# Performance work log

Hardware: AMD Instinct MI355X
Metric: run time of the kernel (lower is better)

Reference implementation:

```python
import jax, jax.numpy as jnp
import numpy as np
from jax import lax

EPS = 1e-8
ROOT_2 = 1.41421
STYLE_SIZE = 512
OUT_CH = 512
STYLE_SCALE = (2.0 / STYLE_SIZE) ** 0.5   # Weight_Scaling(style_size): equalized-LR sqrt(2/fan_in)
OUT_SCALE = (2.0 / (OUT_CH * 1 * 1)) ** 0.5  # Weight_Scaling(out_channels*1*1)


def setup_inputs() -> dict:
    key = jax.random.key(0)
    ks = jax.random.split(key, 10)
    B, Cin, Cout, H, S = 8, 512, 512, 32, 512
    return {
        "x": jax.random.normal(ks[0], (B, Cin, H, H), dtype=jnp.float32),
        "style_base": jax.random.normal(ks[1], (B, S), dtype=jnp.float32),
        "noise": jax.random.normal(ks[2], (B, 1, 2 * H, 2 * H), dtype=jnp.float32),
        "t": jax.random.normal(ks[3], (B, Cout, 2 * H, 2 * H), dtype=jnp.float32),
        # learned params
        "affine_w": jax.random.normal(ks[4], (Cin, S), dtype=jnp.float32) * (1.0 / np.sqrt(S)),
        "affine_b": jnp.zeros((Cin,), dtype=jnp.float32),
        "conv_w": jax.random.normal(ks[5], (Cout, Cin, 3, 3), dtype=jnp.float32),
        "conv_b": jnp.zeros((1, Cout, 1, 1), dtype=jnp.float32),
        "prelu_a": jnp.asarray(0.25, dtype=jnp.float32),
        "noise_scalar": jnp.zeros((1, Cout, 1, 1), dtype=jnp.float32) + 0.1,
        "out_w": jax.random.normal(ks[6], (3, Cout, 1, 1), dtype=jnp.float32) * (1.0 / np.sqrt(Cout)),
        "out_b": jnp.zeros((3,), dtype=jnp.float32),
    }


def reference(x, style_base, noise, t, affine_w, affine_b, conv_w, conv_b,
              prelu_a, noise_scalar, out_w, out_b):
    B, Cin, H, W = x.shape
    # style_std = affine(Weight_Scaling(style_base)) + 1  -> [B, Cin]
    style_std = (style_base * STYLE_SCALE) @ affine_w.T + affine_b + 1.0

    # bilinear x2 upsample (align_corners=False == half-pixel, matches jax.image.resize)
    x = jax.image.resize(x, (B, Cin, 2 * H, 2 * W), method="bilinear")

    # modulated conv with L2 demodulation, expressed as input-scale + conv + output-scale
    # per-sample weight w_b[o,i,k,l] = w[o,i,k,l]*s[b,i] / ||w*s||_b,o
    wsq = jnp.sum(conv_w ** 2, axis=(2, 3))                      # [O, I]
    demod = 1.0 / jnp.sqrt(jnp.einsum("oi,bi->bo", wsq, style_std ** 2) + EPS)  # [B, O]
    xm = x * style_std[:, :, None, None]
    y = lax.conv_general_dilated(xm, conv_w, (1, 1), "SAME",
                                 dimension_numbers=("NCHW", "OIHW", "NCHW"))
    y = y * demod[:, :, None, None] + conv_b + noise_scalar * noise
    # PReLU (single shared slope)
    y = jnp.where(y >= 0, y, prelu_a * y)

    # out branch: skip add, scale, toRGB 1x1 conv, clamp
    y = (y + t) / ROOT_2
    out = lax.conv_general_dilated(y * OUT_SCALE, out_w, (1, 1), "SAME",
                                   dimension_numbers=("NCHW", "OIHW", "NCHW"))
    out = jnp.clip(out + out_b[None, :, None, None], 0.0, 1.0)
    return (y, out)
```

## Files before the change

kernel.cpp:

```cpp
#include <hip/hip_runtime.h>


typedef short bf16x8 __attribute__((ext_vector_type(8)));
typedef short short8v __attribute__((ext_vector_type(8)));
typedef float f32x16 __attribute__((ext_vector_type(16)));

#define WS_STYLE 0
#define WS_DEMOD 16384
#define WS_WSQ   32768
#define WS_WPACK 1081344
#define WS_XM    5799936
#define WS_PART  41484288

__device__ __forceinline__ short f2bf(float f) {
  unsigned u = __float_as_uint(f);
  u += 0x7FFFu + ((u >> 16) & 1u);
  return (short)(u >> 16);
}

__device__ __forceinline__ void gld16(const short* g, char* l) {
  __builtin_amdgcn_global_load_lds((const __attribute__((address_space(1))) void*)g,
                                   (__attribute__((address_space(3))) void*)l,
                                   16, 0, 0);
}

__global__ void k_style(const float* __restrict__ sb, const float* __restrict__ aw,
                        const float* __restrict__ ab, float* __restrict__ style) {
  __shared__ float s_sb[512];
  int b = blockIdx.x;
  for (int i = threadIdx.x; i < 512; i += 256) s_sb[i] = sb[b * 512 + i] * 0.0625f;
  __syncthreads();
  for (int i = threadIdx.x; i < 512; i += 256) {
    const float4* wrow = (const float4*)(aw + (size_t)i * 512);
    float acc = 0.f;
    #pragma unroll 4
    for (int s4 = 0; s4 < 128; ++s4) {
      float4 w4 = wrow[s4];
      float4 sv = *(const float4*)(s_sb + s4 * 4);
      acc += w4.x * sv.x + w4.y * sv.y + w4.z * sv.z + w4.w * sv.w;
    }
    style[b * 512 + i] = acc + ab[i] + 1.0f;
  }
}

__global__ void k_wsq(const float* __restrict__ cw, float* __restrict__ wsq) {
  int idx = blockIdx.x * 256 + threadIdx.x;
  const float* p = cw + (size_t)idx * 9;
  float s = 0.f;
  #pragma unroll
  for (int j = 0; j < 9; ++j) s += p[j] * p[j];
  wsq[idx] = s;
}

__global__ void k_demod(const float* __restrict__ wsq, const float* __restrict__ style,
                        float* __restrict__ demod) {
  int wid = threadIdx.x >> 6, lane = threadIdx.x & 63;
  int idx = blockIdx.x * 4 + wid;
  int b = idx >> 9, o = idx & 511;
  const float* wr = wsq + (size_t)o * 512;
  const float* ss = style + b * 512;
  float sum = 0.f;
  #pragma unroll
  for (int k = 0; k < 8; ++k) {
    int i = k * 64 + lane;
    float s = ss[i];
    sum += wr[i] * s * s;
  }
  #pragma unroll
  for (int off = 32; off; off >>= 1) sum += __shfl_down(sum, off);
  if (lane == 0) demod[b * 512 + o] = rsqrtf(sum + 1e-8f);
}

__global__ void k_upsample(const float* __restrict__ x, const float* __restrict__ style,
                           short* __restrict__ xm) {
  int b = blockIdx.x / 66, hp = blockIdx.x % 66;
  short* xmp = xm + ((size_t)b * 66 + hp) * 66 * 512;
  if (hp == 0 || hp == 65) {
    short8v z = {0, 0, 0, 0, 0, 0, 0, 0};
    for (int u = threadIdx.x; u < 66 * 512 / 8; u += 256) ((short8v*)xmp)[u] = z;
    return;
  }
  int h = hp - 1;
  int j0 = (h >> 1) - 1 + (h & 1);
  float fj = (h & 1) ? 0.25f : 0.75f;
  int j0c = j0 < 0 ? 0 : j0;
  int j1c = j0 + 1 > 31 ? 31 : j0 + 1;
  __shared__ float xt[2][64][33];
  int ccc = threadIdx.x & 63;
  int wsub = threadIdx.x >> 6;
  for (int c0 = 0; c0 < 512; c0 += 64) {
    __syncthreads();
    #pragma unroll 4
    for (int k = 0; k < 16; ++k) {
      int idx = k * 256 + threadIdx.x;
      int ii = idx & 31, cc = (idx >> 5) & 63, jj = idx >> 11;
      xt[jj][cc][ii] = x[(((size_t)b * 512 + c0 + cc) * 32 + (jj ? j1c : j0c)) * 32 + ii];
    }
    __syncthreads();
    float sstyle = style[b * 512 + c0 + ccc];
    #pragma unroll 4
    for (int wk = 0; wk < 16; ++wk) {
      int w = wk * 4 + wsub;
      int i0 = (w >> 1) - 1 + (w & 1);
      float fi = (w & 1) ? 0.25f : 0.75f;
      int i0c = i0 < 0 ? 0 : i0;
      int i1c = i0 + 1 > 31 ? 31 : i0 + 1;
      float v0 = xt[0][ccc][i0c] * (1.f - fi) + xt[0][ccc][i1c] * fi;
      float v1 = xt[1][ccc][i0c] * (1.f - fi) + xt[1][ccc][i1c] * fi;
      float v = (v0 * (1.f - fj) + v1 * fj) * sstyle;
      xmp[(size_t)(w + 1) * 512 + c0 + ccc] = f2bf(v);
    }
    if (wsub == 0) {
      xmp[c0 + ccc] = 0;
      xmp[(size_t)65 * 512 + c0 + ccc] = 0;
    }
  }
}

__global__ void k_packw(const float* __restrict__ cw, short* __restrict__ wpk) {
  int unit = blockIdx.x * 256 + threadIdx.x;
  int s = unit >> 11;
  int rem = unit & 2047;
  int o = rem >> 2, sp = rem & 3;
  int tap = s >> 4, cc = s & 15;
  int i0 = cc * 32 + ((sp ^ ((o >> 1) & 3)) << 3);
  const float* src = cw + ((size_t)o * 512 + i0) * 9 + tap;
  short8v v;
  #pragma unroll
  for (int j = 0; j < 8; ++j) v[j] = f2bf(src[j * 9]);
  *(short8v*)(wpk + (size_t)unit * 8) = v;
}

__global__ __launch_bounds__(256, 2) void k_conv(
    const short* __restrict__ xm, const short* __restrict__ wpk,
    const float* __restrict__ demod, const float* __restrict__ convb,
    const float* __restrict__ nscal, const float* __restrict__ noise,
    const float* __restrict__ t, const float* __restrict__ prelu_a,
    const float* __restrict__ ow, float* __restrict__ part,
    float* __restrict__ y) {
  __shared__ char WTs[6][8192];
  __shared__ char XMb[25344];

  int tid = threadIdx.x;
  int bid = blockIdx.x;
  int coq = bid & 3, hq = (bid >> 2) & 15, b = bid >> 6;
  int wsrow = tid >> 6, lane = tid & 63;
  int l31 = lane & 31, lg = lane >> 5;

  const short* xb = xm + ((size_t)b * 66 + hq * 4) * 66 * 512;
  const short* wpkq = wpk + (size_t)coq * 128 * 32;
  int wb0 = (l31 << 6) + ((lg ^ ((l31 >> 1) & 3)) << 4);

  int off0, off1, off2, off3, off4, off5, off6;
  int d0, d1, d2, d3, d4, d5, d6;
  {
    int u, r, rem, wp, sp;
    u = tid;        r = u / 264; rem = u - r * 264; wp = rem >> 2; sp = rem & 3;
    off0 = (r * 66 + wp) * 512 + ((sp ^ ((wp >> 1) & 3)) << 3); d0 = u * 16;
    u = 256 + tid;  r = u / 264; rem = u - r * 264; wp = rem >> 2; sp = rem & 3;
    off1 = (r * 66 + wp) * 512 + ((sp ^ ((wp >> 1) & 3)) << 3); d1 = u * 16;
    u = 512 + tid;  r = u / 264; rem = u - r * 264; wp = rem >> 2; sp = rem & 3;
    off2 = (r * 66 + wp) * 512 + ((sp ^ ((wp >> 1) & 3)) << 3); d2 = u * 16;
    u = 768 + tid;  r = u / 264; rem = u - r * 264; wp = rem >> 2; sp = rem & 3;
    off3 = (r * 66 + wp) * 512 + ((sp ^ ((wp >> 1) & 3)) << 3); d3 = u * 16;
    u = 1024 + tid; r = u / 264; rem = u - r * 264; wp = rem >> 2; sp = rem & 3;
    off4 = (r * 66 + wp) * 512 + ((sp ^ ((wp >> 1) & 3)) << 3); d4 = u * 16;
    u = 1280 + tid; r = u / 264; rem = u - r * 264; wp = rem >> 2; sp = rem & 3;
    off5 = (r * 66 + wp) * 512 + ((sp ^ ((wp >> 1) & 3)) << 3); d5 = u * 16;
    u = 1536 + (tid & 63); if (u > 1583) u = 1583;
    r = u / 264; rem = u - r * 264; wp = rem >> 2; sp = rem & 3;
    off6 = (r * 66 + wp) * 512 + ((sp ^ ((wp >> 1) & 3)) << 3); d6 = u * 16;
  }

  gld16(xb + off0, XMb + d0);
  gld16(xb + off1, XMb + d1);
  gld16(xb + off2, XMb + d2);
  gld16(xb + off3, XMb + d3);
  gld16(xb + off4, XMb + d4);
  gld16(xb + off5, XMb + d5);
  if (tid < 48) gld16(xb + off6, XMb + d6);
  #pragma unroll
  for (int j = 0; j < 3; ++j) {
    const short* ws = wpkq + (size_t)(j * 16) * 16384;
    gld16(ws + tid * 8, WTs[j] + tid * 16);
    gld16(ws + (256 + tid) * 8, WTs[j] + (256 + tid) * 16);
  }

  f32x16 zf = {0,0,0,0,0,0,0,0,0,0,0,0,0,0,0,0};
  f32x16 acc[4][2];
  #pragma unroll
  for (int i = 0; i < 4; ++i) { acc[i][0] = zf; acc[i][1] = zf; }

  asm volatile("s_waitcnt vmcnt(0)" ::: "memory");
  __builtin_amdgcn_s_barrier();
  __builtin_amdgcn_sched_barrier(0);

  short8v xr0, xr1, xr2, xr3, xr4, xr5, xr6;

  #pragma unroll 1
  for (int cc = 0; cc < 16; ++cc) {
    #pragma unroll
    for (int krow = 0; krow < 3; ++krow) {
      int g = cc * 3 + krow;
      const char* WTc = (const char*)WTs + (size_t)((g & 1) * 3) * 8192;
      char* WTn = (char*)WTs + (size_t)(((g + 1) & 1) * 3) * 8192;

      if (g < 47) {
        int nkrow = (krow < 2) ? krow + 1 : 0;
        int ncc = (krow < 2) ? cc : cc + 1;
        #pragma unroll
        for (int j = 0; j < 3; ++j) {
          const short* ws = wpkq + (size_t)((nkrow * 3 + j) * 16 + ncc) * 16384;
          gld16(ws + tid * 8, WTn + j * 8192 + tid * 16);
          gld16(ws + (256 + tid) * 8, WTn + j * 8192 + (256 + tid) * 16);
        }
      }
      if (krow == 2 && cc < 15) {
        const short* xs = xb + (cc + 1) * 32;
        xr0 = *(const short8v*)(xs + off0);
        xr1 = *(const short8v*)(xs + off1);
        xr2 = *(const short8v*)(xs + off2);
        xr3 = *(const short8v*)(xs + off3);
        xr4 = *(const short8v*)(xs + off4);
        xr5 = *(const short8v*)(xs + off5);
        if (tid < 48) xr6 = *(const short8v*)(xs + off6);
      }

      #pragma unroll
      for (int j = 0; j < 3; ++j) {
        const char* Wp = WTc + j * 8192;
        bf16x8 wf0[4], wf1[4];
        #pragma unroll
        for (int cf = 0; cf < 4; ++cf) {
          wf0[cf] = *(const bf16x8*)(Wp + (wb0 + cf * 2048));
          wf1[cf] = *(const bf16x8*)(Wp + ((wb0 + cf * 2048) ^ 32));
        }
        int a = l31 + j;
        int xo = ((wsrow + krow) * 66 + a) * 64 + ((lg ^ ((a >> 1) & 3)) << 4);
        bf16x8 xf00 = *(const bf16x8*)(XMb + xo);
        bf16x8 xf01 = *(const bf16x8*)(XMb + xo + 2048);
        bf16x8 xf10 = *(const bf16x8*)(XMb + (xo ^ 32));
        bf16x8 xf11 = *(const bf16x8*)(XMb + ((xo ^ 32) + 2048));

        #pragma unroll
        for (int cf = 0; cf < 4; ++cf) {
          acc[cf][0] = __builtin_amdgcn_mfma_f32_32x32x16_bf16(wf0[cf], xf00, acc[cf][0], 0, 0, 0);
          acc[cf][1] = __builtin_amdgcn_mfma_f32_32x32x16_bf16(wf0[cf], xf01, acc[cf][1], 0, 0, 0);
        }
        #pragma unroll
        for (int cf = 0; cf < 4; ++cf) {
          acc[cf][0] = __builtin_amdgcn_mfma_f32_32x32x16_bf16(wf1[cf], xf10, acc[cf][0], 0, 0, 0);
          acc[cf][1] = __builtin_amdgcn_mfma_f32_32x32x16_bf16(wf1[cf], xf11, acc[cf][1], 0, 0, 0);
        }
      }

      if (krow < 2) {
        asm volatile("s_waitcnt vmcnt(0)" ::: "memory");
        __builtin_amdgcn_s_barrier();
        __builtin_amdgcn_sched_barrier(0);
      } else {
        asm volatile("s_waitcnt vmcnt(0) lgkmcnt(0)" ::: "memory");
        __builtin_amdgcn_s_barrier();
        if (cc < 15) {
          *(short8v*)(XMb + d0) = xr0;
          *(short8v*)(XMb + d1) = xr1;
          *(short8v*)(XMb + d2) = xr2;
          *(short8v*)(XMb + d3) = xr3;
          *(short8v*)(XMb + d4) = xr4;
          *(short8v*)(XMb + d5) = xr5;
          if (tid < 48) *(short8v*)(XMb + d6) = xr6;
        }
        asm volatile("s_waitcnt lgkmcnt(0)" ::: "memory");
        __builtin_amdgcn_s_barrier();
        __builtin_amdgcn_sched_barrier(0);
      }
    }
  }

  float pa = prelu_a[0];
  const float inv_r2 = 1.0f / 1.41421f;
  int h = hq * 4 + wsrow;
  float nz0 = noise[((size_t)b * 64 + h) * 64 + l31];
  float nz1 = noise[((size_t)b * 64 + h) * 64 + 32 + l31];
  float pr[3][2] = {{0.f, 0.f}, {0.f, 0.f}, {0.f, 0.f}};
  #pragma unroll
  for (int cf = 0; cf < 4; ++cf) {
    #pragma unroll
    for (int reg = 0; reg < 16; ++reg) {
      int orow = (reg & 3) + 8 * (reg >> 2) + 4 * lg;
      int o = coq * 128 + cf * 32 + orow;
      float dm = demod[b * 512 + o];
      float cb = convb[o];
      float ns = nscal[o];
      float w0 = ow[o], w1 = ow[512 + o], w2 = ow[1024 + o];
      #pragma unroll
      for (int sf = 0; sf < 2; ++sf) {
        int w = sf * 32 + l31;
        float v = acc[cf][sf][reg];
        v = v * dm + cb + ns * (sf ? nz1 : nz0);
        v = (v >= 0.f) ? v : pa * v;
        size_t oi = (((size_t)b * 512 + o) * 64 + h) * 64 + w;
        v = (v + t[oi]) * inv_r2;
        y[oi] = v;
        pr[0][sf] += v * w0;
        pr[1][sf] += v * w1;
        pr[2][sf] += v * w2;
      }
    }
  }
  #pragma unroll
  for (int c = 0; c < 3; ++c) {
    #pragma unroll
    for (int sf = 0; sf < 2; ++sf)
      pr[c][sf] += __shfl_down(pr[c][sf], 32);
  }
  if (lane < 32) {
    int slice = coq;
    float* pp = part + (((size_t)(slice * 8 + b) * 3) * 64 + h) * 64;
    #pragma unroll
    for (int c = 0; c < 3; ++c) {
      #pragma unroll
      for (int sf = 0; sf < 2; ++sf)
        pp[(size_t)c * 4096 + sf * 32 + l31] = pr[c][sf];
    }
  }
}

__global__ void k_rgbfin(const float* __restrict__ part, const float* __restrict__ ob,
                         float* __restrict__ out) {
  int idx = blockIdx.x * 256 + threadIdx.x;
  int c = (idx / 4096) % 3;
  float s = part[idx] + part[98304 + idx] + part[196608 + idx] + part[294912 + idx];
  s = s * 0.0625f + ob[c];
  s = fminf(fmaxf(s, 0.f), 1.f);
  out[idx] = s;
}

extern "C" void kernel_launch(void* const* d_in, const int* in_sizes, int n_in,
                              void* d_out, int out_size, void* d_ws, size_t ws_size,
                              hipStream_t stream) {
  const float* x     = (const float*)d_in[0];
  const float* sb    = (const float*)d_in[1];
  const float* noise = (const float*)d_in[2];
  const float* t     = (const float*)d_in[3];
  const float* aw    = (const float*)d_in[4];
  const float* ab    = (const float*)d_in[5];
  const float* cw    = (const float*)d_in[6];
  const float* cb    = (const float*)d_in[7];
  const float* pa    = (const float*)d_in[8];
  const float* ns    = (const float*)d_in[9];
  const float* ow    = (const float*)d_in[10];
  const float* ob    = (const float*)d_in[11];
  char* ws = (char*)d_ws;
  float* style = (float*)(ws + WS_STYLE);
  float* demod = (float*)(ws + WS_DEMOD);
  float* wsq   = (float*)(ws + WS_WSQ);
  short* wpk   = (short*)(ws + WS_WPACK);
  short* xmw   = (short*)(ws + WS_XM);
  float* part  = (float*)(ws + WS_PART);
  float* y   = (float*)d_out;
  float* out = y + 16777216;

  k_style<<<8, 256, 0, stream>>>(sb, aw, ab, style);
  k_wsq<<<1024, 256, 0, stream>>>(cw, wsq);
  k_demod<<<1024, 256, 0, stream>>>(wsq, style, demod);
  k_upsample<<<528, 256, 0, stream>>>(x, style, xmw);
  k_packw<<<1152, 256, 0, stream>>>(cw, wpk);
  k_conv<<<512, 256, 0, stream>>>(xmw, wpk, demod, cb, ns, noise, t, pa, ow, part, y);
  k_rgbfin<<<384, 256, 0, stream>>>(part, ob, out);
}
```

Baseline: 218.5 us.

## Merge prep kernels, upsample two rows per block, remap conv blocks per XCD

The five preprocessing kernels are folded into two launches: one covers style, wsq and weight packing, and the other covers demod and upsampling. This cuts launch gaps and serialization. The upsample now loads three source rows and produces two output rows per block, so redundant input loads are shared across the pair. The conv block index is remapped so the four output-channel quarters of one (batch, row) tile land on the same XCD, which should improve L2 reuse of the input tile. The cost is more complex per-block branching and higher shared memory use in the upsample part.

```diff
diff --git a/kernel.cpp b/kernel.cpp
--- a/kernel.cpp
+++ b/kernel.cpp
@@ -24,111 +24,131 @@
                                    16, 0, 0);
 }
 
-__global__ void k_style(const float* __restrict__ sb, const float* __restrict__ aw,
-                        const float* __restrict__ ab, float* __restrict__ style) {
+__global__ void k_prep(const float* __restrict__ sb, const float* __restrict__ aw,
+                       const float* __restrict__ ab, const float* __restrict__ cw,
+                       float* __restrict__ style, float* __restrict__ wsq,
+                       short* __restrict__ wpk) {
   __shared__ float s_sb[512];
-  int b = blockIdx.x;
-  for (int i = threadIdx.x; i < 512; i += 256) s_sb[i] = sb[b * 512 + i] * 0.0625f;
-  __syncthreads();
-  for (int i = threadIdx.x; i < 512; i += 256) {
-    const float4* wrow = (const float4*)(aw + (size_t)i * 512);
-    float acc = 0.f;
-    #pragma unroll 4
-    for (int s4 = 0; s4 < 128; ++s4) {
-      float4 w4 = wrow[s4];
-      float4 sv = *(const float4*)(s_sb + s4 * 4);
-      acc += w4.x * sv.x + w4.y * sv.y + w4.z * sv.z + w4.w * sv.w;
-    }
-    style[b * 512 + i] = acc + ab[i] + 1.0f;
-  }
-}
-
-__global__ void k_wsq(const float* __restrict__ cw, float* __restrict__ wsq) {
-  int idx = blockIdx.x * 256 + threadIdx.x;
-  const float* p = cw + (size_t)idx * 9;
-  float s = 0.f;
-  #pragma unroll
-  for (int j = 0; j < 9; ++j) s += p[j] * p[j];
-  wsq[idx] = s;
-}
-
-__global__ void k_demod(const float* __restrict__ wsq, const float* __restrict__ style,
-                        float* __restrict__ demod) {
-  int wid = threadIdx.x >> 6, lane = threadIdx.x & 63;
-  int idx = blockIdx.x * 4 + wid;
-  int b = idx >> 9, o = idx & 511;
-  const float* wr = wsq + (size_t)o * 512;
-  const float* ss = style + b * 512;
-  float sum = 0.f;
-  #pragma unroll
-  for (int k = 0; k < 8; ++k) {
-    int i = k * 64 + lane;
-    float s = ss[i];
-    sum += wr[i] * s * s;
-  }
-  #pragma unroll
-  for (int off = 32; off; off >>= 1) sum += __shfl_down(sum, off);
-  if (lane == 0) demod[b * 512 + o] = rsqrtf(sum + 1e-8f);
-}
-
-__global__ void k_upsample(const float* __restrict__ x, const float* __restrict__ style,
-                           short* __restrict__ xm) {
-  int b = blockIdx.x / 66, hp = blockIdx.x % 66;
-  short* xmp = xm + ((size_t)b * 66 + hp) * 66 * 512;
-  if (hp == 0 || hp == 65) {
-    short8v z = {0, 0, 0, 0, 0, 0, 0, 0};
-    for (int u = threadIdx.x; u < 66 * 512 / 8; u += 256) ((short8v*)xmp)[u] = z;
+  int bid = blockIdx.x, tid = threadIdx.x;
+  if (bid < 8) {
+    int b = bid;
+    for (int i = tid; i < 512; i += 256) s_sb[i] = sb[b * 512 + i] * 0.0625f;
+    __syncthreads();
+    for (int i = tid; i < 512; i += 256) {
+      const float4* wrow = (const float4*)(aw + (size_t)i * 512);
+      float acc = 0.f;
+      #pragma unroll 4
+      for (int s4 = 0; s4 < 128; ++s4) {
+        float4 w4 = wrow[s4];
+        float4 sv = *(const float4*)(s_sb + s4 * 4);
+        acc += w4.x * sv.x + w4.y * sv.y + w4.z * sv.z + w4.w * sv.w;
+      }
+      style[b * 512 + i] = acc + ab[i] + 1.0f;
+    }
+  } else if (bid < 1032) {
+    int idx = (bid - 8) * 256 + tid;
+    const float* p = cw + (size_t)idx * 9;
+    float s = 0.f;
+    #pragma unroll
+    for (int j = 0; j < 9; ++j) s += p[j] * p[j];
+    wsq[idx] = s;
+  } else {
+    int unit = (bid - 1032) * 256 + tid;
+    int s = unit >> 11;
+    int rem = unit & 2047;
+    int o = rem >> 2, sp = rem & 3;
+    int tap = s >> 4, cc = s & 15;
+    int i0 = cc * 32 + ((sp ^ ((o >> 1) & 3)) << 3);
+    const float* src = cw + ((size_t)o * 512 + i0) * 9 + tap;
+    short8v v;
+    #pragma unroll
+    for (int j = 0; j < 8; ++j) v[j] = f2bf(src[j * 9]);
+    *(short8v*)(wpk + (size_t)unit * 8) = v;
+  }
+}
+
+__global__ void k_prep2(const float* __restrict__ wsq, const float* __restrict__ style,
+                        const float* __restrict__ x, float* __restrict__ demod,
+                        short* __restrict__ xm) {
+  __shared__ float xt[3][64][33];
+  int bid = blockIdx.x, tid = threadIdx.x;
+  if (bid < 1024) {
+    int wid = tid >> 6, lane = tid & 63;
+    int idx = bid * 4 + wid;
+    int b = idx >> 9, o = idx & 511;
+    const float* wr = wsq + (size_t)o * 512;
+    const float* ss = style + b * 512;
+    float sum = 0.f;
+    #pragma unroll
+    for (int k = 0; k < 8; ++k) {
+      int i = k * 64 + lane;
+      float s = ss[i];
+      sum += wr[i] * s * s;
+    }
+    #pragma unroll
+    for (int off = 32; off; off >>= 1) sum += __shfl_down(sum, off);
+    if (lane == 0) demod[b * 512 + o] = rsqrtf(sum + 1e-8f);
     return;
   }
-  int h = hp - 1;
-  int j0 = (h >> 1) - 1 + (h & 1);
-  float fj = (h & 1) ? 0.25f : 0.75f;
-  int j0c = j0 < 0 ? 0 : j0;
-  int j1c = j0 + 1 > 31 ? 31 : j0 + 1;
-  __shared__ float xt[2][64][33];
-  int ccc = threadIdx.x & 63;
-  int wsub = threadIdx.x >> 6;
+  int bb = bid - 1024;
+  int b = bb >> 5, k = bb & 31;
+  short* xmp1 = xm + ((size_t)b * 66 + (2 * k + 1)) * 66 * 512;
+  short* xmp2 = xmp1 + 66 * 512;
+  int rm1 = (k > 0) ? k - 1 : 0;
+  int rp1 = (k < 31) ? k + 1 : 31;
+  int cl = tid & 31, wg = tid >> 5;
+  const float* xbb = x + (size_t)b * 512 * 1024;
+
   for (int c0 = 0; c0 < 512; c0 += 64) {
     __syncthreads();
-    #pragma unroll 4
-    for (int k = 0; k < 16; ++k) {
-      int idx = k * 256 + threadIdx.x;
-      int ii = idx & 31, cc = (idx >> 5) & 63, jj = idx >> 11;
-      xt[jj][cc][ii] = x[(((size_t)b * 512 + c0 + cc) * 32 + (jj ? j1c : j0c)) * 32 + ii];
+    #pragma unroll 6
+    for (int tt = 0; tt < 24; ++tt) {
+      int idx = tt * 256 + tid;
+      int r = idx >> 11, rem = idx & 2047;
+      int cc = rem >> 5, ii = rem & 31;
+      int row = (r == 0) ? rm1 : ((r == 1) ? k : rp1);
+      xt[r][cc][ii] = xbb[(size_t)(c0 + cc) * 1024 + row * 32 + ii];
     }
     __syncthreads();
-    float sstyle = style[b * 512 + c0 + ccc];
-    #pragma unroll 4
-    for (int wk = 0; wk < 16; ++wk) {
-      int w = wk * 4 + wsub;
+    int ca = c0 + 2 * cl;
+    float2 sv = *(const float2*)(style + b * 512 + ca);
+    #pragma unroll
+    for (int p = 0; p < 8; ++p) {
+      int w = wg * 8 + p;
       int i0 = (w >> 1) - 1 + (w & 1);
       float fi = (w & 1) ? 0.25f : 0.75f;
       int i0c = i0 < 0 ? 0 : i0;
-      int i1c = i0 + 1 > 31 ? 31 : i0 + 1;
-      float v0 = xt[0][ccc][i0c] * (1.f - fi) + xt[0][ccc][i1c] * fi;
-      float v1 = xt[1][ccc][i0c] * (1.f - fi) + xt[1][ccc][i1c] * fi;
-      float v = (v0 * (1.f - fj) + v1 * fj) * sstyle;
-      xmp[(size_t)(w + 1) * 512 + c0 + ccc] = f2bf(v);
-    }
-    if (wsub == 0) {
-      xmp[c0 + ccc] = 0;
-      xmp[(size_t)65 * 512 + c0 + ccc] = 0;
-    }
-  }
-}
-
-__global__ void k_packw(const float* __restrict__ cw, short* __restrict__ wpk) {
-  int unit = blockIdx.x * 256 + threadIdx.x;
-  int s = unit >> 11;
-  int rem = unit & 2047;
-  int o = rem >> 2, sp = rem & 3;
-  int tap = s >> 4, cc = s & 15;
-  int i0 = cc * 32 + ((sp ^ ((o >> 1) & 3)) << 3);
-  const float* src = cw + ((size_t)o * 512 + i0) * 9 + tap;
-  short8v v;
-  #pragma unroll
-  for (int j = 0; j < 8; ++j) v[j] = f2bf(src[j * 9]);
-  *(short8v*)(wpk + (size_t)unit * 8) = v;
+      int i1c = (i0 + 1 > 31) ? 31 : i0 + 1;
+      float gi = 1.f - fi;
+      float h0a = xt[0][2 * cl][i0c] * gi + xt[0][2 * cl][i1c] * fi;
+      float h1a = xt[1][2 * cl][i0c] * gi + xt[1][2 * cl][i1c] * fi;
+      float h2a = xt[2][2 * cl][i0c] * gi + xt[2][2 * cl][i1c] * fi;
+      float h0b = xt[0][2 * cl + 1][i0c] * gi + xt[0][2 * cl + 1][i1c] * fi;
+      float h1b = xt[1][2 * cl + 1][i0c] * gi + xt[1][2 * cl + 1][i1c] * fi;
+      float h2b = xt[2][2 * cl + 1][i0c] * gi + xt[2][2 * cl + 1][i1c] * fi;
+      short2 o1, o2;
+      o1.x = f2bf((0.25f * h0a + 0.75f * h1a) * sv.x);
+      o1.y = f2bf((0.25f * h0b + 0.75f * h1b) * sv.y);
+      o2.x = f2bf((0.75f * h1a + 0.25f * h2a) * sv.x);
+      o2.y = f2bf((0.75f * h1b + 0.25f * h2b) * sv.y);
+      *(short2*)(xmp1 + (size_t)(w + 1) * 512 + ca) = o1;
+      *(short2*)(xmp2 + (size_t)(w + 1) * 512 + ca) = o2;
+    }
+    if (tid < 64)       xmp1[c0 + tid] = 0;
+    else if (tid < 128) xmp1[(size_t)65 * 512 + c0 + (tid - 64)] = 0;
+    else if (tid < 192) xmp2[c0 + (tid - 128)] = 0;
+    else                xmp2[(size_t)65 * 512 + c0 + (tid - 192)] = 0;
+  }
+  if (k == 0) {
+    short8v z = {0, 0, 0, 0, 0, 0, 0, 0};
+    short* xmp0 = xm + (size_t)b * 66 * 66 * 512;
+    for (int u = tid; u < 66 * 512 / 8; u += 256) ((short8v*)xmp0)[u] = z;
+  }
+  if (k == 31) {
+    short8v z = {0, 0, 0, 0, 0, 0, 0, 0};
+    short* xmp65 = xm + ((size_t)b * 66 + 65) * 66 * 512;
+    for (int u = tid; u < 66 * 512 / 8; u += 256) ((short8v*)xmp65)[u] = z;
+  }
 }
 
 __global__ __launch_bounds__(256, 2) void k_conv(
@@ -143,7 +163,10 @@
 
   int tid = threadIdx.x;
   int bid = blockIdx.x;
-  int coq = bid & 3, hq = (bid >> 2) & 15, b = bid >> 6;
+  int xcd = bid & 7, q = bid >> 3;
+  int coq = q & 3, ghi = q >> 2;
+  int g5 = ghi * 8 + xcd;
+  int hq = g5 & 15, b = g5 >> 4;
   int wsrow = tid >> 6, lane = tid & 63;
   int l31 = lane & 31, lg = lane >> 5;
 
@@ -361,11 +384,8 @@
   float* y   = (float*)d_out;
   float* out = y + 16777216;
 
-  k_style<<<8, 256, 0, stream>>>(sb, aw, ab, style);
-  k_wsq<<<1024, 256, 0, stream>>>(cw, wsq);
-  k_demod<<<1024, 256, 0, stream>>>(wsq, style, demod);
-  k_upsample<<<528, 256, 0, stream>>>(x, style, xmw);
-  k_packw<<<1152, 256, 0, stream>>>(cw, wpk);
+  k_prep<<<2184, 256, 0, stream>>>(sb, aw, ab, cw, style, wsq, wpk);
+  k_prep2<<<1280, 256, 0, stream>>>(wsq, style, x, demod, xmw);
   k_conv<<<512, 256, 0, stream>>>(xmw, wpk, demod, cb, ns, noise, t, pa, ow, part, y);
   k_rgbfin<<<384, 256, 0, stream>>>(part, ob, out);
 }
```

After: 229.0 us. 1.05x slower.
